# Optimization experiments

Hardware: AMD Instinct MI355X
Metric: run time of the kernel (lower is better)

Reference implementation:

```python
import jax, jax.numpy as jnp
import numpy as np

N = 50000
E = 800000
D_IN = 128
D_H = 128
N_CLASSES = 2


def gcn_conv(x, W, b, src, dst, n):
    # x: [n, d_in]; src/dst: [E+n] edge endpoints WITH self loops already appended
    h = x @ W  # [n, d_out]
    ones = jnp.ones(src.shape[0], dtype=x.dtype)
    deg = jax.ops.segment_sum(ones, dst, num_segments=n)  # in-degree incl. self loop
    inv_sqrt = jnp.where(deg > 0, jax.lax.rsqrt(deg), 0.0)
    norm = inv_sqrt[src] * inv_sqrt[dst]  # [E+n]
    msg = h[src] * norm[:, None]  # gather + scale, [E+n, d_out]
    out = jax.ops.segment_sum(msg, dst, num_segments=n)  # scatter-add
    return out + b


def setup_inputs() -> dict:
    key = jax.random.key(0)
    ks = jax.random.split(key, 8)
    x = jax.random.normal(ks[0], (N, D_IN), dtype=jnp.float32)
    edge_index = jax.random.randint(ks[1], (2, E), 0, N, dtype=jnp.int64)
    s1 = 1.0 / np.sqrt(D_IN)
    s2 = 1.0 / np.sqrt(D_H)
    W1 = jax.random.uniform(ks[2], (D_IN, D_H), jnp.float32, -s1, s1)
    b1 = jnp.zeros((D_H,), jnp.float32)
    W2 = jax.random.uniform(ks[3], (D_H, D_H), jnp.float32, -s2, s2)
    b2 = jnp.zeros((D_H,), jnp.float32)
    Wc = jax.random.uniform(ks[4], (D_H, N_CLASSES), jnp.float32, -s2, s2)
    bc = jnp.zeros((N_CLASSES,), jnp.float32)
    return {"x": x, "edge_index": edge_index, "W1": W1, "b1": b1,
            "W2": W2, "b2": b2, "Wc": Wc, "bc": bc}


def reference(x, edge_index, W1, b1, W2, b2, Wc, bc):
    n = x.shape[0]
    # add self loops (GCNConv default)
    loops = jnp.arange(n, dtype=edge_index.dtype)
    src = jnp.concatenate([edge_index[0], loops])
    dst = jnp.concatenate([edge_index[1], loops])
    h = jax.nn.relu(gcn_conv(x, W1, b1, src, dst, n))
    # dropout is identity in eval mode
    h = jax.nn.relu(gcn_conv(h, W2, b2, src, dst, n))
    logits = h @ Wc + bc
    return logits
```

## Files before the change

kernel.cpp:

```cpp
#include <hip/hip_runtime.h>

#define DH 128
#define ELLW 64

typedef __attribute__((ext_vector_type(8))) short short8;
typedef __attribute__((ext_vector_type(4))) float f32x4;

__device__ inline unsigned f2bf(float f) {
    unsigned b = __float_as_uint(f);
    b += 0x7fff + ((b >> 16) & 1);
    return b >> 16;
}
__device__ inline float bflo(unsigned u) { return __uint_as_float(u << 16); }
__device__ inline float bfhi(unsigned u) { return __uint_as_float(u & 0xffff0000u); }

__global__ __launch_bounds__(256) void k_zero_int(int* __restrict__ p, int n) {
    int i = blockIdx.x * 256 + threadIdx.x;
    if (i < n) p[i] = 0;
}

__global__ __launch_bounds__(256) void k_fill(const int* __restrict__ src,
                                              const int* __restrict__ dst,
                                              int* __restrict__ cnt,
                                              unsigned* __restrict__ ell,
                                              int nE, int ns) {
    int grp = blockIdx.x & 7;
    int blk = blockIdx.x >> 3;
    int nblk = gridDim.x >> 3;
    int lo = grp * ns, hi = lo + ns;
    for (int e = blk * 256 + threadIdx.x; e < nE; e += nblk * 256) {
        int d = dst[e];
        if (d >= lo && d < hi) {
            int slot = atomicAdd(&cnt[d], 1);
            if (slot < ELLW) ell[(size_t)d * ELLW + slot] = (unsigned)src[e];
        }
    }
}

__global__ __launch_bounds__(256) void k_inv(const int* __restrict__ cnt,
                                             float* __restrict__ inv, int n) {
    int i = blockIdx.x * 256 + threadIdx.x;
    if (i < n) inv[i] = rsqrtf((float)(cnt[i] + 1));
}

template <int AF32>
__global__ __launch_bounds__(256) void k_gemm_mfma(const void* __restrict__ Avoid,
                                                   const float* __restrict__ W,
                                                   unsigned* __restrict__ Cp, int n) {
    __shared__ unsigned Wl[64 * 128];
    int tid = threadIdx.x;

    for (int i = tid; i < 128 * 64; i += 256) {
        int c = i & 127;
        int k = (i >> 7) * 2;
        float w0 = W[(size_t)k * DH + c];
        float w1 = W[(size_t)(k + 1) * DH + c];
        unsigned pk = f2bf(w0) | (f2bf(w1) << 16);
        int ua = c * 64 + ((((k >> 3) + c) & 15) << 2) + ((k & 7) >> 1);
        Wl[ua] = pk;
    }
    __syncthreads();

    int wid = tid >> 6, lane = tid & 63;
    int q = lane >> 4;
    int row0 = blockIdx.x * 64 + wid * 16;
    int r = row0 + (lane & 15);
    int rl = min(r, n - 1);

    short8 af[4];
    if (AF32) {
        const float* A = (const float*)Avoid;
#pragma unroll
        for (int ks = 0; ks < 4; ++ks) {
            const float* ap = &A[(size_t)rl * DH + ks * 32 + q * 8];
            float4 fa = *(const float4*)ap;
            float4 fb = *(const float4*)(ap + 4);
            short8 a;
            a[0] = (short)f2bf(fa.x); a[1] = (short)f2bf(fa.y);
            a[2] = (short)f2bf(fa.z); a[3] = (short)f2bf(fa.w);
            a[4] = (short)f2bf(fb.x); a[5] = (short)f2bf(fb.y);
            a[6] = (short)f2bf(fb.z); a[7] = (short)f2bf(fb.w);
            af[ks] = a;
        }
    } else {
        const unsigned* Ap = (const unsigned*)Avoid;
#pragma unroll
        for (int ks = 0; ks < 4; ++ks)
            af[ks] = *(const short8*)&Ap[(size_t)rl * 64 + ks * 16 + q * 4];
    }

    f32x4 acc[8];
#pragma unroll
    for (int cb = 0; cb < 8; ++cb) acc[cb] = (f32x4){0.f, 0.f, 0.f, 0.f};

#pragma unroll
    for (int cb = 0; cb < 8; ++cb) {
        int c = cb * 16 + (lane & 15);
#pragma unroll
        for (int ks = 0; ks < 4; ++ks) {
            int k0 = ks * 32 + q * 8;
            int ua = c * 64 + ((((k0 >> 3) + c) & 15) << 2);
            short8 bf = *(const short8*)&Wl[ua];
            acc[cb] = __builtin_amdgcn_mfma_f32_16x16x32_bf16(af[ks], bf, acc[cb], 0, 0, 0);
        }
    }

    __syncthreads();
    float* Cl = (float*)Wl;
#pragma unroll
    for (int cb = 0; cb < 8; ++cb) {
        int col = cb * 16 + (lane & 15);
#pragma unroll
        for (int reg = 0; reg < 4; ++reg) {
            int lrow = wid * 16 + q * 4 + reg;
            Cl[lrow * DH + col] = acc[cb][reg];
        }
    }
    __syncthreads();

    int base = blockIdx.x * 64;
    for (int i = tid; i < 64 * 64; i += 256) {
        int lrow = i >> 6, cu = i & 63;
        int grow = base + lrow;
        if (grow < n) {
            float v0 = Cl[lrow * DH + cu * 2];
            float v1 = Cl[lrow * DH + cu * 2 + 1];
            Cp[(size_t)grow * 64 + cu] = f2bf(v0) | (f2bf(v1) << 16);
        }
    }
}

template <int FUSE_CLS>
__global__ __launch_bounds__(256) void k_gather(const unsigned* __restrict__ hp,
                                                const unsigned* __restrict__ ell,
                                                const int* __restrict__ cnt,
                                                const float* __restrict__ inv,
                                                const float* __restrict__ bias,
                                                unsigned* __restrict__ outp,
                                                const float* __restrict__ Wc,
                                                const float* __restrict__ bc,
                                                float* __restrict__ logits, int n) {
    int node = (blockIdx.x * 256 + threadIdx.x) >> 4;
    int lq = threadIdx.x & 15;
    if (node >= n) return;

    int deg = min(cnt[node], ELLW);
    const unsigned* erow = &ell[(size_t)node * ELLW];
    float vi = inv[node];
    float sl = vi * vi;

    uint4 hs = *(const uint4*)&hp[(size_t)node * 64 + lq * 4];
    float ax[8];
    ax[0] = bflo(hs.x) * sl; ax[1] = bfhi(hs.x) * sl;
    ax[2] = bflo(hs.y) * sl; ax[3] = bfhi(hs.y) * sl;
    ax[4] = bflo(hs.z) * sl; ax[5] = bfhi(hs.z) * sl;
    ax[6] = bflo(hs.w) * sl; ax[7] = bfhi(hs.w) * sl;

    int j = 0;
    for (; j + 4 <= deg; j += 4) {
        unsigned s[4];
        float nf[4];
        uint4 u[4];
#pragma unroll
        for (int k = 0; k < 4; ++k) s[k] = erow[j + k];
#pragma unroll
        for (int k = 0; k < 4; ++k) nf[k] = inv[s[k]] * vi;
#pragma unroll
        for (int k = 0; k < 4; ++k)
            u[k] = *(const uint4*)&hp[(size_t)s[k] * 64 + lq * 4];
#pragma unroll
        for (int k = 0; k < 4; ++k) {
            ax[0] = fmaf(bflo(u[k].x), nf[k], ax[0]);
            ax[1] = fmaf(bfhi(u[k].x), nf[k], ax[1]);
            ax[2] = fmaf(bflo(u[k].y), nf[k], ax[2]);
            ax[3] = fmaf(bfhi(u[k].y), nf[k], ax[3]);
            ax[4] = fmaf(bflo(u[k].z), nf[k], ax[4]);
            ax[5] = fmaf(bfhi(u[k].z), nf[k], ax[5]);
            ax[6] = fmaf(bflo(u[k].w), nf[k], ax[6]);
            ax[7] = fmaf(bfhi(u[k].w), nf[k], ax[7]);
        }
    }
    for (; j < deg; ++j) {
        unsigned s = erow[j];
        float nf = inv[s] * vi;
        uint4 u = *(const uint4*)&hp[(size_t)s * 64 + lq * 4];
        ax[0] = fmaf(bflo(u.x), nf, ax[0]);
        ax[1] = fmaf(bfhi(u.x), nf, ax[1]);
        ax[2] = fmaf(bflo(u.y), nf, ax[2]);
        ax[3] = fmaf(bfhi(u.y), nf, ax[3]);
        ax[4] = fmaf(bflo(u.z), nf, ax[4]);
        ax[5] = fmaf(bfhi(u.z), nf, ax[5]);
        ax[6] = fmaf(bflo(u.w), nf, ax[6]);
        ax[7] = fmaf(bfhi(u.w), nf, ax[7]);
    }

    float4 b0 = *(const float4*)&bias[lq * 8];
    float4 b1 = *(const float4*)&bias[lq * 8 + 4];
    ax[0] = fmaxf(ax[0] + b0.x, 0.f); ax[1] = fmaxf(ax[1] + b0.y, 0.f);
    ax[2] = fmaxf(ax[2] + b0.z, 0.f); ax[3] = fmaxf(ax[3] + b0.w, 0.f);
    ax[4] = fmaxf(ax[4] + b1.x, 0.f); ax[5] = fmaxf(ax[5] + b1.y, 0.f);
    ax[6] = fmaxf(ax[6] + b1.z, 0.f); ax[7] = fmaxf(ax[7] + b1.w, 0.f);

    if (!FUSE_CLS) {
        uint4 o;
        o.x = f2bf(ax[0]) | (f2bf(ax[1]) << 16);
        o.y = f2bf(ax[2]) | (f2bf(ax[3]) << 16);
        o.z = f2bf(ax[4]) | (f2bf(ax[5]) << 16);
        o.w = f2bf(ax[6]) | (f2bf(ax[7]) << 16);
        *(uint4*)&outp[(size_t)node * 64 + lq * 4] = o;
    } else {
        float p0 = 0.f, p1 = 0.f;
#pragma unroll
        for (int m = 0; m < 4; ++m) {
            float4 w = *(const float4*)&Wc[lq * 16 + m * 4];
            p0 += ax[2 * m] * w.x + ax[2 * m + 1] * w.z;
            p1 += ax[2 * m] * w.y + ax[2 * m + 1] * w.w;
        }
#pragma unroll
        for (int off = 8; off > 0; off >>= 1) {
            p0 += __shfl_down(p0, off);
            p1 += __shfl_down(p1, off);
        }
        if (lq == 0) {
            logits[(size_t)node * 2 + 0] = p0 + bc[0];
            logits[(size_t)node * 2 + 1] = p1 + bc[1];
        }
    }
}

extern "C" void kernel_launch(void* const* d_in, const int* in_sizes, int n_in,
                              void* d_out, int out_size, void* d_ws, size_t ws_size,
                              hipStream_t stream) {
    const float* x  = (const float*)d_in[0];
    const int*   ei = (const int*)d_in[1];
    const float* W1 = (const float*)d_in[2];
    const float* b1 = (const float*)d_in[3];
    const float* W2 = (const float*)d_in[4];
    const float* b2 = (const float*)d_in[5];
    const float* Wc = (const float*)d_in[6];
    const float* bc = (const float*)d_in[7];
    float* out = (float*)d_out;

    int n  = in_sizes[0] / DH;
    int nE = in_sizes[1] / 2;
    const int* src = ei;
    const int* dst = ei + nE;

    size_t o = 0;
    auto alloc = [&](size_t bytes) {
        size_t r = o;
        o = (o + bytes + 255) & ~(size_t)255;
        return r;
    };
    char* ws = (char*)d_ws;
    int*      cnt = (int*)(ws + alloc((size_t)n * 4));
    float*    inv = (float*)(ws + alloc((size_t)n * 4));
    unsigned* ell = (unsigned*)(ws + alloc((size_t)n * ELLW * 4));
    unsigned* hpA = (unsigned*)(ws + alloc((size_t)n * 64 * 4));
    unsigned* hpB = (unsigned*)(ws + alloc((size_t)n * 64 * 4));

    int nB = (n + 255) / 256;
    int gemmB = (n + 63) / 64;
    int gatherB = (n + 15) / 16;
    int ns = (n + 7) / 8;

    k_zero_int<<<nB, 256, 0, stream>>>(cnt, n);
    k_fill<<<2048, 256, 0, stream>>>(src, dst, cnt, ell, nE, ns);
    k_inv<<<nB, 256, 0, stream>>>(cnt, inv, n);

    k_gemm_mfma<1><<<gemmB, 256, 0, stream>>>(x, W1, hpA, n);
    k_gather<0><<<gatherB, 256, 0, stream>>>(hpA, ell, cnt, inv, b1, hpB,
                                             nullptr, nullptr, nullptr, n);

    k_gemm_mfma<0><<<gemmB, 256, 0, stream>>>(hpB, W2, hpA, n);
    k_gather<1><<<gatherB, 256, 0, stream>>>(hpA, ell, cnt, inv, b2, nullptr,
                                             Wc, bc, out, n);
}
```

Before: 140.9 us.

## Reorder gather nodes by degree via counting sort; vectorize weight staging

Adds histogram, scan and ordering kernels that bucket nodes by in-degree, so each gather wave processes nodes with similar neighbor counts instead of arbitrary ones. The aim is to cut lane divergence and tail imbalance in the ELL gather loops. The GEMM weight staging also switches to float4 global loads. The cost is three extra kernel launches, heavily contended atomics on 65 bucket counters, and less locality for the self-row reads and output writes, which are now scattered by the permutation.

```diff
diff --git a/kernel.cpp b/kernel.cpp
--- a/kernel.cpp
+++ b/kernel.cpp
@@ -13,6 +13,15 @@
 }
 __device__ inline float bflo(unsigned u) { return __uint_as_float(u << 16); }
 __device__ inline float bfhi(unsigned u) { return __uint_as_float(u & 0xffff0000u); }
+
+__device__ inline int wave_incl_scan(int v, int lane) {
+#pragma unroll
+    for (int off = 1; off < 64; off <<= 1) {
+        int u = __shfl_up(v, off);
+        if (lane >= off) v += u;
+    }
+    return v;
+}
 
 __global__ __launch_bounds__(256) void k_zero_int(int* __restrict__ p, int n) {
     int i = blockIdx.x * 256 + threadIdx.x;
@@ -43,6 +52,37 @@
     if (i < n) inv[i] = rsqrtf((float)(cnt[i] + 1));
 }
 
+__global__ __launch_bounds__(256) void k_hist(const int* __restrict__ cnt,
+                                              int* __restrict__ hist, int n) {
+    __shared__ int lh[65];
+    if (threadIdx.x < 65) lh[threadIdx.x] = 0;
+    __syncthreads();
+    int i = blockIdx.x * 256 + threadIdx.x;
+    if (i < n) atomicAdd(&lh[min(cnt[i], ELLW)], 1);
+    __syncthreads();
+    if (threadIdx.x < 65 && lh[threadIdx.x]) atomicAdd(&hist[threadIdx.x], lh[threadIdx.x]);
+}
+
+__global__ __launch_bounds__(64) void k_hscan(const int* __restrict__ hist,
+                                              int* __restrict__ bcur) {
+    int lane = threadIdx.x;
+    int v = hist[lane];
+    int incl = wave_incl_scan(v, lane);
+    bcur[lane] = incl - v;
+    if (lane == 63) bcur[64] = incl;
+}
+
+__global__ __launch_bounds__(256) void k_ord(const int* __restrict__ cnt,
+                                             int* __restrict__ bcur,
+                                             int* __restrict__ ord, int n) {
+    int i = blockIdx.x * 256 + threadIdx.x;
+    if (i < n) {
+        int d = min(cnt[i], ELLW);
+        int pos = atomicAdd(&bcur[d], 1);
+        ord[pos] = i;
+    }
+}
+
 template <int AF32>
 __global__ __launch_bounds__(256) void k_gemm_mfma(const void* __restrict__ Avoid,
                                                    const float* __restrict__ W,
@@ -50,14 +90,20 @@
     __shared__ unsigned Wl[64 * 128];
     int tid = threadIdx.x;
 
-    for (int i = tid; i < 128 * 64; i += 256) {
-        int c = i & 127;
-        int k = (i >> 7) * 2;
-        float w0 = W[(size_t)k * DH + c];
-        float w1 = W[(size_t)(k + 1) * DH + c];
-        unsigned pk = f2bf(w0) | (f2bf(w1) << 16);
-        int ua = c * 64 + ((((k >> 3) + c) & 15) << 2) + ((k & 7) >> 1);
-        Wl[ua] = pk;
+    for (int i = tid; i < 2048; i += 256) {
+        int c4 = (i & 31) * 4;
+        int k = (i >> 5) * 2;
+        float4 fa = *(const float4*)&W[(size_t)k * DH + c4];
+        float4 fb = *(const float4*)&W[(size_t)(k + 1) * DH + c4];
+        int kb = (k >> 3), ksub = (k & 7) >> 1;
+#pragma unroll
+        for (int t = 0; t < 4; ++t) {
+            int c = c4 + t;
+            float a = (t == 0) ? fa.x : (t == 1) ? fa.y : (t == 2) ? fa.z : fa.w;
+            float b = (t == 0) ? fb.x : (t == 1) ? fb.y : (t == 2) ? fb.z : fb.w;
+            int ua = c * 64 + (((kb + c) & 15) << 2) + ksub;
+            Wl[ua] = f2bf(a) | (f2bf(b) << 16);
+        }
     }
     __syncthreads();
 
@@ -135,14 +181,16 @@
                                                 const unsigned* __restrict__ ell,
                                                 const int* __restrict__ cnt,
                                                 const float* __restrict__ inv,
+                                                const int* __restrict__ ord,
                                                 const float* __restrict__ bias,
                                                 unsigned* __restrict__ outp,
                                                 const float* __restrict__ Wc,
                                                 const float* __restrict__ bc,
                                                 float* __restrict__ logits, int n) {
-    int node = (blockIdx.x * 256 + threadIdx.x) >> 4;
+    int gq = (blockIdx.x * 256 + threadIdx.x) >> 4;
     int lq = threadIdx.x & 15;
-    if (node >= n) return;
+    if (gq >= n) return;
+    int node = ord[gq];
 
     int deg = min(cnt[node], ELLW);
     const unsigned* erow = &ell[(size_t)node * ELLW];
@@ -253,26 +301,37 @@
         return r;
     };
     char* ws = (char*)d_ws;
-    int*      cnt = (int*)(ws + alloc((size_t)n * 4));
-    float*    inv = (float*)(ws + alloc((size_t)n * 4));
-    unsigned* ell = (unsigned*)(ws + alloc((size_t)n * ELLW * 4));
-    unsigned* hpA = (unsigned*)(ws + alloc((size_t)n * 64 * 4));
-    unsigned* hpB = (unsigned*)(ws + alloc((size_t)n * 64 * 4));
-
+    size_t cnt_off = alloc((size_t)n * 4);
+    size_t hist_off = alloc(65 * 4);
+    size_t bcur_off = alloc(65 * 4);
+    int*      cnt  = (int*)(ws + cnt_off);
+    int*      hist = (int*)(ws + hist_off);
+    int*      bcur = (int*)(ws + bcur_off);
+    float*    inv  = (float*)(ws + alloc((size_t)n * 4));
+    int*      ord  = (int*)(ws + alloc((size_t)n * 4));
+    unsigned* ell  = (unsigned*)(ws + alloc((size_t)n * ELLW * 4));
+    unsigned* hpA  = (unsigned*)(ws + alloc((size_t)n * 64 * 4));
+    unsigned* hpB  = (unsigned*)(ws + alloc((size_t)n * 64 * 4));
+
+    int zInts = (int)((bcur_off - cnt_off) / 4) + 65;
     int nB = (n + 255) / 256;
+    int zB = (zInts + 255) / 256;
     int gemmB = (n + 63) / 64;
     int gatherB = (n + 15) / 16;
     int ns = (n + 7) / 8;
 
-    k_zero_int<<<nB, 256, 0, stream>>>(cnt, n);
+    k_zero_int<<<zB, 256, 0, stream>>>(cnt, zInts);
     k_fill<<<2048, 256, 0, stream>>>(src, dst, cnt, ell, nE, ns);
     k_inv<<<nB, 256, 0, stream>>>(cnt, inv, n);
+    k_hist<<<nB, 256, 0, stream>>>(cnt, hist, n);
+    k_hscan<<<1, 64, 0, stream>>>(hist, bcur);
+    k_ord<<<nB, 256, 0, stream>>>(cnt, bcur, ord, n);
 
     k_gemm_mfma<1><<<gemmB, 256, 0, stream>>>(x, W1, hpA, n);
-    k_gather<0><<<gatherB, 256, 0, stream>>>(hpA, ell, cnt, inv, b1, hpB,
+    k_gather<0><<<gatherB, 256, 0, stream>>>(hpA, ell, cnt, inv, ord, b1, hpB,
                                              nullptr, nullptr, nullptr, n);
 
     k_gemm_mfma<0><<<gemmB, 256, 0, stream>>>(hpB, W2, hpA, n);
-    k_gather<1><<<gatherB, 256, 0, stream>>>(hpA, ell, cnt, inv, b2, nullptr,
+    k_gather<1><<<gatherB, 256, 0, stream>>>(hpA, ell, cnt, inv, ord, b2, nullptr,
                                              Wc, bc, out, n);
 }
```

Result: slower. 285.9 us (+103.0%).
